# Kernel tuning notes

Hardware: AMD Instinct MI355X
Metric: run time of the kernel (lower is better)

Reference implementation:

```python
import jax, jax.numpy as jnp
from jax import lax
import numpy as np

EPS = 1e-5  # BatchNorm eps (eval mode, fresh running stats: mean=0, var=1)

N, T, H, C = 16, 512, 64, 64
O, K, E = 64, 9, 256


def setup_inputs() -> dict:
    key = jax.random.key(0)
    ks = jax.random.split(key, 16)
    X = jax.random.normal(ks[0], (N, T, H, C), dtype=jnp.float32)
    edges = jax.random.randint(ks[1], (N, 2, E), 0, H, dtype=jnp.int64)
    # att1/att2: Conv2d(C,1,1) == dot over channels + bias
    w_att1 = jax.random.normal(ks[2], (C,), jnp.float32) * (1.0 / np.sqrt(C))
    b_att1 = jax.random.normal(ks[3], (), jnp.float32) * 0.01
    w_att2 = jax.random.normal(ks[4], (C,), jnp.float32) * (1.0 / np.sqrt(C))
    b_att2 = jax.random.normal(ks[5], (), jnp.float32) * 0.01
    # GCN linear
    W_lin = jax.random.normal(ks[6], (O, C), jnp.float32) * (1.0 / np.sqrt(C))
    b_lin = jax.random.normal(ks[7], (O,), jnp.float32) * 0.01
    # tcn: BN -> ReLU -> Conv2d(O,O,(K,1)) -> BN -> Dropout(eval=id)
    bn1_gamma = 1.0 + 0.1 * jax.random.normal(ks[8], (O,), jnp.float32)
    bn1_beta = 0.1 * jax.random.normal(ks[9], (O,), jnp.float32)
    W_tcn = jax.random.normal(ks[10], (O, O, K, 1), jnp.float32) * (1.0 / np.sqrt(O * K))
    b_tcn = jax.random.normal(ks[11], (O,), jnp.float32) * 0.01
    bn2_gamma = 1.0 + 0.1 * jax.random.normal(ks[12], (O,), jnp.float32)
    bn2_beta = 0.1 * jax.random.normal(ks[13], (O,), jnp.float32)
    return dict(X=X, edges=edges, w_att1=w_att1, b_att1=b_att1, w_att2=w_att2,
                b_att2=b_att2, W_lin=W_lin, b_lin=b_lin, bn1_gamma=bn1_gamma,
                bn1_beta=bn1_beta, W_tcn=W_tcn, b_tcn=b_tcn,
                bn2_gamma=bn2_gamma, bn2_beta=bn2_beta)


def _bn_eval(x, gamma, beta):
    # eval-mode BatchNorm2d with running_mean=0, running_var=1; x is (N, Cc, T, H)
    inv = gamma / jnp.sqrt(1.0 + EPS)
    return x * inv[None, :, None, None] + beta[None, :, None, None]


def _forward(X, edges, w_att1, b_att1, w_att2, b_att2, W_lin, b_lin,
             bn1_gamma, bn1_beta, W_tcn, b_tcn, bn2_gamma, bn2_beta):
    n, t, h, c = X.shape
    k = W_tcn.shape[2]
    # --- adjacency from edge lists (duplicates sum, as sparse_coo->to_dense) ---
    bidx = jnp.arange(n)[:, None]
    adj = jnp.zeros((n, h, h), X.dtype).at[bidx, edges[:, 0, :], edges[:, 1, :]].add(1.0)
    # --- attention: a1[n,t,h] + a2[n,t,h'], leaky_relu, softmax over h ---
    a1 = jnp.einsum('nthc,c->nth', X, w_att1) + b_att1
    a2 = jnp.einsum('nthc,c->nth', X, w_att2) + b_att2
    s = jax.nn.leaky_relu(a1[:, :, :, None] + a2[:, :, None, :], 0.01)  # (n,t,h,h')
    att = jax.nn.softmax(s, axis=2)  # softmax over h (dim=1 pre-permute)
    # --- GCN: einsum('nthh,ntho->ntho') only uses diag(adj@att + I) ---
    diag = jnp.einsum('nhk,ntkh->nth', adj, att) + 1.0
    support = jnp.einsum('nthc,oc->ntho', X, W_lin) + b_lin  # (n,t,h,O)
    g = diag[..., None] * support
    # --- tcn: BN -> ReLU -> temporal conv (K,1) -> BN -> Dropout(eval) ---
    y = jnp.transpose(g, (0, 3, 1, 2))  # (n,O,t,h)
    y = jax.nn.relu(_bn_eval(y, bn1_gamma, bn1_beta))
    pad = (k - 1) // 2
    y = lax.conv_general_dilated(y, W_tcn, window_strides=(1, 1),
                                 padding=[(pad, pad), (0, 0)])
    y = y + b_tcn[None, :, None, None]
    y = _bn_eval(y, bn2_gamma, bn2_beta)
    # --- residual (identity: in==out, stride=1) + relu ---
    y = y + jnp.transpose(X, (0, 3, 1, 2))
    return jnp.transpose(jax.nn.relu(y), (0, 2, 3, 1))  # (n,t,h,O)


def reference(X, edges, w_att1, b_att1, w_att2, b_att2, W_lin, b_lin,
              bn1_gamma, bn1_beta, W_tcn, b_tcn, bn2_gamma, bn2_beta):
    return _forward(X, edges, w_att1, b_att1, w_att2, b_att2, W_lin, b_lin,
                    bn1_gamma, bn1_beta, W_tcn, b_tcn, bn2_gamma, bn2_beta)
```

## Files before the change

### kernel.cpp

```cpp
#include <hip/hip_runtime.h>
#include <hip/hip_bf16.h>
#include <stdint.h>

typedef float f32x4 __attribute__((ext_vector_type(4)));
typedef __bf16 bf16x8 __attribute__((ext_vector_type(8)));
typedef __bf16 bf16x4 __attribute__((ext_vector_type(4)));
typedef unsigned short u16;
typedef unsigned int u32;

__device__ __forceinline__ u16 f2bf(float f) {
    u32 u = __float_as_uint(f);
    u32 r = (u + 0x7fffu + ((u >> 16) & 1u)) >> 16;
    return (u16)r;
}

template <int CTRL>
__device__ __forceinline__ float rrot(float x) {
    int r = __builtin_amdgcn_update_dpp(0, __builtin_bit_cast(int, x), CTRL, 0xF, 0xF, false);
    return __builtin_bit_cast(float, r);
}
__device__ __forceinline__ float rowsum16(float p) {
    p += rrot<0x128>(p);
    p += rrot<0x124>(p);
    p += rrot<0x122>(p);
    p += rrot<0x121>(p);
    return p;
}

#define NB_ATTN 2048

__global__ __launch_bounds__(256) void k_attn(
    const float* __restrict__ X, const int* __restrict__ edges,
    const float* __restrict__ w1g, const float* __restrict__ b1g,
    const float* __restrict__ w2g, const float* __restrict__ b2g,
    const float* __restrict__ Wlin, const float* __restrict__ Wtcn,
    const float* __restrict__ blin, const float* __restrict__ g1,
    const float* __restrict__ be1, const float* __restrict__ btcn,
    const float* __restrict__ g2, const float* __restrict__ be2,
    u16* __restrict__ wlin_p, u16* __restrict__ wtcn_p,
    float* __restrict__ aux, float* __restrict__ diag) {
    const int tid = threadIdx.x;
    const int bid = blockIdx.x;
    const float rsf = 1.0f / sqrtf(1.0f + 1e-5f);

    if (bid >= NB_ATTN) {
        int idx = (bid - NB_ATTN) * 256 + tid;
        if (idx < 4096) {
            int jj = idx & 7, l = (idx >> 3) & 63, j = (idx >> 9) & 3, s = idx >> 11;
            int o = j * 16 + (l & 15);
            int c = s * 32 + (l >> 4) * 8 + jj;
            wlin_p[idx] = f2bf(Wlin[o * 64 + c] * (g1[o] * rsf));
        }
        int i2 = idx - 4096;
        if (i2 >= 0 && i2 < 36864) {
            int jj = i2 & 7, l = (i2 >> 3) & 63, j = (i2 >> 9) & 3, s = (i2 >> 11) & 1, kk = i2 >> 12;
            int o = j * 16 + (l & 15);
            int op = s * 32 + (l >> 4) * 8 + jj;
            wtcn_p[i2] = f2bf(Wtcn[(o * 64 + op) * 9 + kk] * (g2[o] * rsf));
        }
        if (idx >= 40960 && tid < 64) {
            aux[tid] = blin[tid] * g1[tid] * rsf;
            aux[64 + tid] = be1[tid];
            aux[128 + tid] = btcn[tid] * g2[tid] * rsf + be2[tid];
        }
        return;
    }

    __shared__ __align__(16) float adjT[64 * 65];
    __shared__ __align__(16) float A1s[4][64], A2s[4][64];

    const int n = bid >> 7;
    const int tg = bid & 127;
    const int w = tid >> 6, l = tid & 63;
    const int t = tg * 4 + w;
    const int c4 = l & 15, q = l >> 4;

    {
        f32x4 z4 = {0.f, 0.f, 0.f, 0.f};
        for (int i = tid; i < 1040; i += 256) *(f32x4*)(&adjT[i * 4]) = z4;
    }
    __syncthreads();
    {
        int r = edges[n * 512 + tid];
        int c = edges[n * 512 + 256 + tid];
        atomicAdd(&adjT[c * 65 + r], 1.0f);
    }

    const float* Xt = X + (size_t)(n * 512 + t) * 4096;
    const float4 w1v = *(const float4*)(w1g + c4 * 4);
    const float4 w2v = *(const float4*)(w2g + c4 * 4);
    float a1h = 0.f, a2h = 0.f;
#pragma unroll 8
    for (int i = 0; i < 16; i++) {
        float4 xv = *(const float4*)(Xt + (i * 64 + l) * 4);
        float p1 = xv.x * w1v.x + xv.y * w1v.y + xv.z * w1v.z + xv.w * w1v.w;
        float p2 = xv.x * w2v.x + xv.y * w2v.y + xv.z * w2v.z + xv.w * w2v.w;
        p1 = rowsum16(p1);
        p2 = rowsum16(p2);
        if (c4 == i) { a1h = p1; a2h = p2; }
    }
    {
        int hh = c4 * 4 + q;
        A1s[w][hh] = a1h + b1g[0];
        A2s[w][hh] = a2h + b2g[0];
    }
    __syncthreads();

    {
        float a2 = A2s[w][l];
        float num = 0.f, den = 0.f;
#pragma unroll
        for (int k4 = 0; k4 < 16; k4++) {
            float4 a1v = *(const float4*)(&A1s[w][k4 * 4]);
#pragma unroll
            for (int j = 0; j < 4; j++) {
                int k = k4 * 4 + j;
                float s = ((const float*)&a1v)[j] + a2;
                s = fmaxf(s, 0.01f * s);
                float e = __expf(s);
                den += e;
                num = fmaf(adjT[k * 65 + l], e, num);
            }
        }
        diag[((size_t)(n * 64 + l)) * 512 + t] = num / den + 1.0f;
    }
}

__global__ __launch_bounds__(256, 4) void k_gcn_tcn(
    const float* __restrict__ X, const float* __restrict__ diag,
    const u16* __restrict__ wlin_p, const u16* __restrict__ wtcn_p,
    const float* __restrict__ aux, float* __restrict__ out) {
    __shared__ __align__(16) u16 As[272 * 72];
    __shared__ float DGs[272];

    const int tid = threadIdx.x;
    const int bid = blockIdx.x;
    const int n = bid >> 7, h = (bid >> 1) & 63, tb = (bid & 1) * 256;
    const float* Xbase = X + ((size_t)(n * 512) * 64 + h) * 64;

    const int w = tid >> 6, l = tid & 63;
    const int col = l & 15, q = l >> 4;
    const f32x4 zv = {0.f, 0.f, 0.f, 0.f};

    float blp[4], bb1[4], cc2[4];
#pragma unroll
    for (int j = 0; j < 4; j++) {
        int o = 16 * j + col;
        blp[j] = aux[o];
        bb1[j] = aux[64 + o];
        cc2[j] = aux[128 + o];
    }
#pragma unroll
    for (int i = 0; i < 2; i++) {
        int idx = tid + 256 * i;
        if (idx < 272) {
            int tg = tb - 4 + idx;
            DGs[idx] = (tg >= 0 && tg < 512) ? diag[((size_t)(n * 64 + h)) * 512 + tg] : 0.f;
        }
    }

#pragma unroll
    for (int i = 0; i < 17; i++) {
        int idx = tid + 256 * i;
        int r = idx >> 4, c4 = idx & 15;
        int tg = tb - 4 + r;
        float4 xv = make_float4(0.f, 0.f, 0.f, 0.f);
        if (tg >= 0 && tg < 512) xv = *(const float4*)(Xbase + (size_t)tg * 4096 + c4 * 4);
        bf16x4 pk;
        pk[0] = (__bf16)xv.x; pk[1] = (__bf16)xv.y;
        pk[2] = (__bf16)xv.z; pk[3] = (__bf16)xv.w;
        *(bf16x4*)(&As[r * 72 + c4 * 4]) = pk;
    }
    __syncthreads();

    for (int mt = w; mt < 17; mt += 4) {
        f32x4 acc[4] = {zv, zv, zv, zv};
#pragma unroll
        for (int s = 0; s < 2; s++) {
            bf16x8 a = *(const bf16x8*)(&As[(16 * mt + col) * 72 + s * 32 + q * 8]);
#pragma unroll
            for (int j = 0; j < 4; j++) {
                bf16x8 b = *(const bf16x8*)(&wlin_p[((s * 4 + j) * 64 + l) * 8]);
                acc[j] = __builtin_amdgcn_mfma_f32_16x16x32_bf16(a, b, acc[j], 0, 0, 0);
            }
        }
#pragma unroll
        for (int j = 0; j < 4; j++) {
#pragma unroll
            for (int rr = 0; rr < 4; rr++) {
                int row = 16 * mt + q * 4 + rr;
                int tg = tb - 4 + row;
                float v = fmaf(acc[j][rr] + blp[j], DGs[row], bb1[j]);
                v = v > 0.f ? v : 0.f;
                if (tg < 0 || tg >= 512) v = 0.f;
                __bf16 bv = (__bf16)v;
                As[row * 72 + 16 * j + col] = __builtin_bit_cast(u16, bv);
            }
        }
    }
    __syncthreads();

    f32x4 acc2[4][4];
#pragma unroll
    for (int mt = 0; mt < 4; mt++)
#pragma unroll
        for (int j = 0; j < 4; j++) acc2[mt][j] = zv;

    for (int kk = 0; kk < 9; kk++) {
#pragma unroll
        for (int s = 0; s < 2; s++) {
            bf16x8 b[4];
#pragma unroll
            for (int j = 0; j < 4; j++)
                b[j] = *(const bf16x8*)(&wtcn_p[(((kk * 2 + s) * 4 + j) * 64 + l) * 8]);
#pragma unroll
            for (int mt = 0; mt < 4; mt++) {
                bf16x8 a = *(const bf16x8*)(&As[(64 * w + 16 * mt + col + kk) * 72 + s * 32 + q * 8]);
#pragma unroll
                for (int j = 0; j < 4; j++)
                    acc2[mt][j] = __builtin_amdgcn_mfma_f32_16x16x32_bf16(a, b[j], acc2[mt][j], 0, 0, 0);
            }
        }
    }

#pragma unroll
    for (int mt = 0; mt < 4; mt++) {
        float res[4][4];
#pragma unroll
        for (int rr = 0; rr < 4; rr++) {
            int tt = tb + 64 * w + 16 * mt + 4 * q + rr;
#pragma unroll
            for (int j = 0; j < 4; j++)
                res[j][rr] = X[((size_t)(n * 512 + tt) * 64 + h) * 64 + 16 * j + col];
        }
#pragma unroll
        for (int rr = 0; rr < 4; rr++) {
            int tt = tb + 64 * w + 16 * mt + 4 * q + rr;
#pragma unroll
            for (int j = 0; j < 4; j++) {
                size_t off = ((size_t)(n * 512 + tt) * 64 + h) * 64 + 16 * j + col;
                float v = acc2[mt][j][rr] + cc2[j] + res[j][rr];
                out[off] = v > 0.f ? v : 0.f;
            }
        }
    }
}

extern "C" void kernel_launch(void* const* d_in, const int* in_sizes, int n_in,
                              void* d_out, int out_size, void* d_ws, size_t ws_size,
                              hipStream_t stream) {
    const float* X    = (const float*)d_in[0];
    const int*  edges = (const int*)d_in[1];
    const float* w1   = (const float*)d_in[2];
    const float* b1   = (const float*)d_in[3];
    const float* w2   = (const float*)d_in[4];
    const float* b2   = (const float*)d_in[5];
    const float* Wlin = (const float*)d_in[6];
    const float* blin = (const float*)d_in[7];
    const float* g1   = (const float*)d_in[8];
    const float* be1  = (const float*)d_in[9];
    const float* Wtcn = (const float*)d_in[10];
    const float* btcn = (const float*)d_in[11];
    const float* g2   = (const float*)d_in[12];
    const float* be2  = (const float*)d_in[13];
    float* out = (float*)d_out;

    char* ws = (char*)d_ws;
    u16*   wlin_p = (u16*)ws;
    u16*   wtcn_p = (u16*)(ws + 8192);
    float* aux    = (float*)(ws + 8192 + 73728);
    float* diag   = (float*)(ws + 8192 + 73728 + 1024);

    hipLaunchKernelGGL(k_attn, dim3(NB_ATTN + 161), dim3(256), 0, stream,
                       X, edges, w1, b1, w2, b2, Wlin, Wtcn,
                       blin, g1, be1, btcn, g2, be2,
                       wlin_p, wtcn_p, aux, diag);
    hipLaunchKernelGGL(k_gcn_tcn, dim3(16 * 64 * 2), dim3(256), 0, stream,
                       X, diag, wlin_p, wtcn_p, aux, out);
}
```

Before: 308.7 us.

## Halve attention grid, hoist GCN weights to registers, double-buffer residual loads

The attention kernel now handles eight timesteps per block in two passes, so the adjacency build per block is amortised over twice the work and the grid shrinks to 1024 blocks. The GCN weight fragments are loaded once into registers instead of being re-read inside the M-tile loop. The epilogue prefetches residual X tiles one step ahead with two register buffers, so global loads overlap with output stores. This raises register pressure in the fused kernel and removes the barrier between the A1s/A2s writes and reads, which is only safe because each wavefront uses its own slice.

```diff
diff --git a/kernel.cpp b/kernel.cpp
--- a/kernel.cpp
+++ b/kernel.cpp
@@ -27,7 +27,7 @@
     return p;
 }
 
-#define NB_ATTN 2048
+#define NB_ATTN 1024
 
 __global__ __launch_bounds__(256) void k_attn(
     const float* __restrict__ X, const int* __restrict__ edges,
@@ -69,10 +69,9 @@
     __shared__ __align__(16) float adjT[64 * 65];
     __shared__ __align__(16) float A1s[4][64], A2s[4][64];
 
-    const int n = bid >> 7;
-    const int tg = bid & 127;
+    const int n = bid >> 6;
+    const int tg = bid & 63;
     const int w = tid >> 6, l = tid & 63;
-    const int t = tg * 4 + w;
     const int c4 = l & 15, q = l >> 4;
 
     {
@@ -85,44 +84,47 @@
         int c = edges[n * 512 + 256 + tid];
         atomicAdd(&adjT[c * 65 + r], 1.0f);
     }
-
-    const float* Xt = X + (size_t)(n * 512 + t) * 4096;
+    __syncthreads();
+
     const float4 w1v = *(const float4*)(w1g + c4 * 4);
     const float4 w2v = *(const float4*)(w2g + c4 * 4);
-    float a1h = 0.f, a2h = 0.f;
+
+    for (int half = 0; half < 2; half++) {
+        const int t = tg * 8 + half * 4 + w;
+        const float* Xt = X + (size_t)(n * 512 + t) * 4096;
+        float a1h = 0.f, a2h = 0.f;
 #pragma unroll 8
-    for (int i = 0; i < 16; i++) {
-        float4 xv = *(const float4*)(Xt + (i * 64 + l) * 4);
-        float p1 = xv.x * w1v.x + xv.y * w1v.y + xv.z * w1v.z + xv.w * w1v.w;
-        float p2 = xv.x * w2v.x + xv.y * w2v.y + xv.z * w2v.z + xv.w * w2v.w;
-        p1 = rowsum16(p1);
-        p2 = rowsum16(p2);
-        if (c4 == i) { a1h = p1; a2h = p2; }
-    }
-    {
-        int hh = c4 * 4 + q;
-        A1s[w][hh] = a1h + b1g[0];
-        A2s[w][hh] = a2h + b2g[0];
-    }
-    __syncthreads();
-
-    {
-        float a2 = A2s[w][l];
-        float num = 0.f, den = 0.f;
-#pragma unroll
-        for (int k4 = 0; k4 < 16; k4++) {
-            float4 a1v = *(const float4*)(&A1s[w][k4 * 4]);
-#pragma unroll
-            for (int j = 0; j < 4; j++) {
-                int k = k4 * 4 + j;
-                float s = ((const float*)&a1v)[j] + a2;
-                s = fmaxf(s, 0.01f * s);
-                float e = __expf(s);
-                den += e;
-                num = fmaf(adjT[k * 65 + l], e, num);
+        for (int i = 0; i < 16; i++) {
+            float4 xv = *(const float4*)(Xt + (i * 64 + l) * 4);
+            float p1 = xv.x * w1v.x + xv.y * w1v.y + xv.z * w1v.z + xv.w * w1v.w;
+            float p2 = xv.x * w2v.x + xv.y * w2v.y + xv.z * w2v.z + xv.w * w2v.w;
+            p1 = rowsum16(p1);
+            p2 = rowsum16(p2);
+            if (c4 == i) { a1h = p1; a2h = p2; }
+        }
+        {
+            int hh = c4 * 4 + q;
+            A1s[w][hh] = a1h + b1g[0];
+            A2s[w][hh] = a2h + b2g[0];
+        }
+        {
+            float a2 = A2s[w][l];
+            float num = 0.f, den = 0.f;
+#pragma unroll
+            for (int k4 = 0; k4 < 16; k4++) {
+                float4 a1v = *(const float4*)(&A1s[w][k4 * 4]);
+#pragma unroll
+                for (int j = 0; j < 4; j++) {
+                    int k = k4 * 4 + j;
+                    float s = ((const float*)&a1v)[j] + a2;
+                    s = fmaxf(s, 0.01f * s);
+                    float e = __expf(s);
+                    den += e;
+                    num = fmaf(adjT[k * 65 + l], e, num);
+                }
             }
-        }
-        diag[((size_t)(n * 64 + l)) * 512 + t] = num / den + 1.0f;
+            diag[((size_t)(n * 64 + l)) * 512 + t] = num / den + 1.0f;
+        }
     }
 }
 
@@ -141,6 +143,11 @@
     const int w = tid >> 6, l = tid & 63;
     const int col = l & 15, q = l >> 4;
     const f32x4 zv = {0.f, 0.f, 0.f, 0.f};
+
+    bf16x8 wb[8];
+#pragma unroll
+    for (int sj = 0; sj < 8; sj++)
+        wb[sj] = *(const bf16x8*)(&wlin_p[(sj * 64 + l) * 8]);
 
     float blp[4], bb1[4], cc2[4];
 #pragma unroll
@@ -179,10 +186,8 @@
         for (int s = 0; s < 2; s++) {
             bf16x8 a = *(const bf16x8*)(&As[(16 * mt + col) * 72 + s * 32 + q * 8]);
 #pragma unroll
-            for (int j = 0; j < 4; j++) {
-                bf16x8 b = *(const bf16x8*)(&wlin_p[((s * 4 + j) * 64 + l) * 8]);
-                acc[j] = __builtin_amdgcn_mfma_f32_16x16x32_bf16(a, b, acc[j], 0, 0, 0);
-            }
+            for (int j = 0; j < 4; j++)
+                acc[j] = __builtin_amdgcn_mfma_f32_16x16x32_bf16(a, wb[s * 4 + j], acc[j], 0, 0, 0);
         }
 #pragma unroll
         for (int j = 0; j < 4; j++) {
@@ -223,27 +228,36 @@
         }
     }
 
-#pragma unroll
-    for (int mt = 0; mt < 4; mt++) {
-        float res[4][4];
-#pragma unroll
-        for (int rr = 0; rr < 4; rr++) {
-            int tt = tb + 64 * w + 16 * mt + 4 * q + rr;
-#pragma unroll
-            for (int j = 0; j < 4; j++)
-                res[j][rr] = X[((size_t)(n * 512 + tt) * 64 + h) * 64 + 16 * j + col];
-        }
-#pragma unroll
-        for (int rr = 0; rr < 4; rr++) {
-            int tt = tb + 64 * w + 16 * mt + 4 * q + rr;
-#pragma unroll
-            for (int j = 0; j < 4; j++) {
-                size_t off = ((size_t)(n * 512 + tt) * 64 + h) * 64 + 16 * j + col;
-                float v = acc2[mt][j][rr] + cc2[j] + res[j][rr];
-                out[off] = v > 0.f ? v : 0.f;
-            }
-        }
-    }
+    float rb0[4][4], rb1[4][4];
+#define ISSUE_RES(dst, mt_)                                                    \
+    {                                                                          \
+        _Pragma("unroll") for (int rr = 0; rr < 4; rr++) {                     \
+            int tt = tb + 64 * w + 16 * (mt_) + 4 * q + rr;                    \
+            _Pragma("unroll") for (int j = 0; j < 4; j++)                      \
+                dst[j][rr] = X[((size_t)(n * 512 + tt) * 64 + h) * 64 + 16 * j + col]; \
+        }                                                                      \
+    }
+#define STORE_MT(R, mt_)                                                       \
+    {                                                                          \
+        _Pragma("unroll") for (int rr = 0; rr < 4; rr++) {                     \
+            int tt = tb + 64 * w + 16 * (mt_) + 4 * q + rr;                    \
+            _Pragma("unroll") for (int j = 0; j < 4; j++) {                    \
+                size_t off = ((size_t)(n * 512 + tt) * 64 + h) * 64 + 16 * j + col; \
+                float v = acc2[mt_][j][rr] + cc2[j] + R[j][rr];                \
+                out[off] = v > 0.f ? v : 0.f;                                  \
+            }                                                                  \
+        }                                                                      \
+    }
+    ISSUE_RES(rb0, 0)
+    ISSUE_RES(rb1, 1)
+    STORE_MT(rb0, 0)
+    ISSUE_RES(rb0, 2)
+    STORE_MT(rb1, 1)
+    ISSUE_RES(rb1, 3)
+    STORE_MT(rb0, 2)
+    STORE_MT(rb1, 3)
+#undef ISSUE_RES
+#undef STORE_MT
 }
 
 extern "C" void kernel_launch(void* const* d_in, const int* in_sizes, int n_in,
```

After: 310.6 us. About the same (+0.6%).
